# Performance work log

Hardware: AMD Instinct MI355X
Metric: run time of the kernel (lower is better)

The kernel has to match this reference:

```python
import jax, jax.numpy as jnp
import numpy as np

B, S, E, H = 4, 2048, 1024, 16
D = E // H  # head dim = 64


def setup_inputs() -> dict:
    key = jax.random.key(0)
    ks = jax.random.split(key, 5)
    s = 0.02
    return {
        "x": jax.random.normal(ks[0], (B, S, E), dtype=jnp.float32),
        "Wq": jax.random.normal(ks[1], (E, E), dtype=jnp.float32) * s,
        "Wk": jax.random.normal(ks[2], (E, E), dtype=jnp.float32) * s,
        "Wv": jax.random.normal(ks[3], (E, E), dtype=jnp.float32) * s,
        "Wo": jax.random.normal(ks[4], (E, E), dtype=jnp.float32) * s,
        "bo": jnp.zeros((E,), dtype=jnp.float32),
    }


def reference(x, Wq, Wk, Wv, Wo, bo):
    b, s, e = x.shape
    h, d = H, e // H
    # QKV projections -> [b, h, s, d]
    q = (x @ Wq).reshape(b, s, h, d).transpose(0, 2, 1, 3)
    k = (x @ Wk).reshape(b, s, h, d).transpose(0, 2, 1, 3)
    v = (x @ Wv).reshape(b, s, h, d).transpose(0, 2, 1, 3)
    # scores [b, h, s, s], causal mask with -inf, scaled softmax
    a = jnp.einsum('bhqd,bhkd->bhqk', q, k)
    causal = jnp.tril(jnp.ones((s, s), dtype=bool))  # True where allowed
    a = jnp.where(causal, a, -jnp.inf) / jnp.sqrt(jnp.asarray(d, x.dtype))
    a = jax.nn.softmax(a, axis=-1)
    # dropout p=0.0 (identity in eval)
    y = jnp.einsum('bhqk,bhkd->bhqd', a, v)
    y = y.transpose(0, 2, 1, 3).reshape(b, s, e)
    return y @ Wo + bo
```

## Files before the change

kernel.cpp:

```cpp
#include <hip/hip_runtime.h>

typedef __bf16 bf16x8 __attribute__((ext_vector_type(8)));
typedef float f32x4 __attribute__((ext_vector_type(4)));
typedef unsigned short u16x8 __attribute__((ext_vector_type(8)));

#define S_LEN 2048
#define NHEAD 16
#define HDIM  64
#define EMB   1024

__device__ __forceinline__ ushort f2b(float v) {
  union { float f; unsigned u; } x; x.f = v;
  unsigned r = (x.u + 0x7fffu + ((x.u >> 16) & 1u)) >> 16;
  return (ushort)r;
}

__device__ __forceinline__ ushort f2b_trunc(float v) {
  union { float f; unsigned u; } x; x.f = v;
  return (ushort)(x.u >> 16);
}

typedef const __attribute__((address_space(1))) unsigned int* gp1_t;
typedef __attribute__((address_space(3))) unsigned int* lp3_t;
__device__ __forceinline__ void gld16(const ushort* g, const ushort* l) {
  __builtin_amdgcn_global_load_lds((gp1_t)(unsigned long long)(uintptr_t)g,
                                   (lp3_t)(unsigned int)(uintptr_t)l, 16, 0, 0);
}

__device__ __forceinline__ void barf() {
  asm volatile("" ::: "memory");
  __builtin_amdgcn_s_barrier();
  asm volatile("" ::: "memory");
}

__global__ __launch_bounds__(256) void prep_kernel(
    const float* __restrict__ x, const float* __restrict__ W0,
    const float* __restrict__ W1, const float* __restrict__ W2,
    const float* __restrict__ W3, ushort* __restrict__ xb,
    ushort* __restrict__ Wt0, ushort* __restrict__ Wt1,
    ushort* __restrict__ Wt2, ushort* __restrict__ Wt3, float scale0) {
  const int z = blockIdx.z;
  if (z == 4) {
    size_t base = ((size_t)(blockIdx.y * 32 + blockIdx.x)) * 8192 + threadIdx.x * 4;
#pragma unroll
    for (int i = 0; i < 8; ++i) {
      float4 v = *(const float4*)(x + base + i * 1024);
      ushort4 o;
      o.x = f2b(v.x); o.y = f2b(v.y); o.z = f2b(v.z); o.w = f2b(v.w);
      *(ushort4*)(xb + base + i * 1024) = o;
    }
    return;
  }
  __shared__ float t[32][33];
  const float* W = z == 0 ? W0 : (z == 1 ? W1 : (z == 2 ? W2 : W3));
  ushort* Wt = z == 0 ? Wt0 : (z == 1 ? Wt1 : (z == 2 ? Wt2 : Wt3));
  const float scale = z == 0 ? scale0 : 1.0f;
  int k0 = blockIdx.x * 32, n0 = blockIdx.y * 32;
  int c = threadIdx.x & 31, r0 = threadIdx.x >> 5;
#pragma unroll
  for (int i = 0; i < 4; ++i) {
    int r = r0 + i * 8;
    t[r][c] = W[(size_t)(k0 + r) * EMB + n0 + c];
  }
  __syncthreads();
#pragma unroll
  for (int i = 0; i < 4; ++i) {
    int r = r0 + i * 8;
    Wt[(size_t)(n0 + r) * EMB + k0 + c] = f2b(t[c][r] * scale);
  }
}

template <int EPI>
__global__ __launch_bounds__(512, 2) void gemm8_kernel(
    const ushort* __restrict__ A, const ushort* __restrict__ Bt,
    ushort* __restrict__ outQ, ushort* __restrict__ outK, ushort* __restrict__ outVt,
    float* __restrict__ outF, const float* __restrict__ bias) {
  __shared__ ushort lds8[73728];
  const int tid = threadIdx.x;
  const int wave = tid >> 6, lane = tid & 63, ln = lane & 15, quad = lane >> 4;
  const int wm = wave >> 2, wn = wave & 3;
  const long m0 = (long)blockIdx.x * 128, n0 = (long)blockIdx.y * 256;
  constexpr int K = EMB, KT = K / 64;

  const int srow = tid >> 3;
  const int scol = ((tid & 7) ^ (srow & 7)) * 8;
  const ushort* srcA = A + (m0 + srow) * (long)K + scol;
  const ushort* srcB = Bt + (n0 + srow) * (long)K + scol;

#define STG_A(t, s)                                                            \
  do {                                                                         \
    gld16(srcA + (t) * 64,               lds8 + (s) * 8192 + tid * 8);         \
    gld16(srcA + (t) * 64 + 64 * K,      lds8 + (s) * 8192 + 4096 + tid * 8);  \
  } while (0)
#define STG_B(t, s)                                                            \
  do {                                                                         \
    gld16(srcB + (t) * 64,               lds8 + 24576 + (s) * 16384 + tid * 8);         \
    gld16(srcB + (t) * 64 + 64 * K,      lds8 + 24576 + (s) * 16384 + 4096 + tid * 8);  \
    gld16(srcB + (t) * 64 + 128 * K,     lds8 + 24576 + (s) * 16384 + 8192 + tid * 8);  \
    gld16(srcB + (t) * 64 + 192 * K,     lds8 + 24576 + (s) * 16384 + 12288 + tid * 8); \
  } while (0)

  const int sw = (ln & 7) * 8;

#define RD_A(kk, s)                                                            \
  do {                                                                         \
    const ushort* p_ = lds8 + (s) * 8192 + (wm * 64 + ln) * 64 +               \
                       (((kk) * 32 + quad * 8) ^ sw);                          \
    af[0] = *(const bf16x8*)p_;                                                \
    af[1] = *(const bf16x8*)(p_ + 1024);                                       \
    af[2] = *(const bf16x8*)(p_ + 2048);                                       \
    af[3] = *(const bf16x8*)(p_ + 3072);                                       \
  } while (0)
#define RD_B(kk, s)                                                            \
  do {                                                                         \
    const ushort* p_ = lds8 + 24576 + (s) * 16384 + (wn * 64 + ln) * 64 +      \
                       (((kk) * 32 + quad * 8) ^ sw);                          \
    bfr[0] = *(const bf16x8*)p_;                                               \
    bfr[1] = *(const bf16x8*)(p_ + 1024);                                      \
    bfr[2] = *(const bf16x8*)(p_ + 2048);                                      \
    bfr[3] = *(const bf16x8*)(p_ + 3072);                                      \
  } while (0)

#define MM16()                                                                 \
  do {                                                                         \
    _Pragma("unroll") for (int mt = 0; mt < 4; ++mt)                           \
        _Pragma("unroll") for (int nt = 0; nt < 4; ++nt)                       \
            acc[mt][nt] = __builtin_amdgcn_mfma_f32_16x16x32_bf16(             \
                af[mt], bfr[nt], acc[mt][nt], 0, 0, 0);                        \
  } while (0)

  STG_A(0, 0); STG_B(0, 0);
  STG_A(1, 1); STG_B(1, 1);
  asm volatile("s_waitcnt vmcnt(6)" ::: "memory");
  barf();

  f32x4 acc[4][4] = {};
  bf16x8 af[4], bfr[4];

#define TILE(t, s, sn)                                                         \
  do {                                                                         \
    RD_A(0, s); RD_B(0, s);                                                    \
    if ((t) + 2 < KT) STG_A((t) + 2, sn);                                      \
    barf();                                                                    \
    __builtin_amdgcn_s_setprio(1);                                             \
    MM16();                                                                    \
    __builtin_amdgcn_s_setprio(0);                                             \
    barf();                                                                    \
    RD_A(1, s); RD_B(1, s);                                                    \
    if ((t) + 2 < KT) STG_B((t) + 2, sn);                                      \
    barf();                                                                    \
    __builtin_amdgcn_s_setprio(1);                                             \
    MM16();                                                                    \
    __builtin_amdgcn_s_setprio(0);                                             \
    if ((t) + 2 < KT) {                                                        \
      asm volatile("s_waitcnt vmcnt(6)" ::: "memory");                         \
    } else if ((t) + 1 < KT) {                                                 \
      asm volatile("s_waitcnt vmcnt(0)" ::: "memory");                         \
    }                                                                          \
    barf();                                                                    \
  } while (0)

  for (int th = 0; th < 15; th += 3) {
    TILE(th, 0, 2);
    TILE(th + 1, 1, 0);
    TILE(th + 2, 2, 1);
  }
  TILE(15, 0, 2);

  if (EPI == 0) {
    const int sel = (int)(n0 >> 10);
    if (sel == 2) {
#pragma unroll
      for (int mt = 0; mt < 4; ++mt) {
        const long mbase = m0 + wm * 64 + mt * 16 + quad * 4;
        const long bb = mbase >> 11, s = mbase & 2047;
#pragma unroll
        for (int nt = 0; nt < 4; ++nt) {
          const int nn = (int)((n0 & 1023) + wn * 64 + nt * 16 + ln);
          const int h = nn >> 6, d = nn & 63;
          uint2 val;
          val.x = (unsigned)f2b(acc[mt][nt][0]) | ((unsigned)f2b(acc[mt][nt][1]) << 16);
          val.y = (unsigned)f2b(acc[mt][nt][2]) | ((unsigned)f2b(acc[mt][nt][3]) << 16);
          *(uint2*)(outVt + (((bb * NHEAD + h) * (long)HDIM + d) * S_LEN) + s) = val;
        }
      }
    } else {
      ushort* dst = sel == 0 ? outQ : outK;
#pragma unroll
      for (int mt = 0; mt < 4; ++mt) {
#pragma unroll
        for (int nt = 0; nt < 4; ++nt) {
          const int nn = (int)((n0 & 1023) + wn * 64 + nt * 16 + ln);
          const int h = nn >> 6, d = nn & 63;
#pragma unroll
          for (int r = 0; r < 4; ++r) {
            const long m = m0 + wm * 64 + mt * 16 + quad * 4 + r;
            const long bb = m >> 11, s = m & 2047;
            dst[(((bb * NHEAD + h) * S_LEN) + s) * HDIM + d] = f2b(acc[mt][nt][r]);
          }
        }
      }
    }
  } else {
#pragma unroll
    for (int mt = 0; mt < 4; ++mt) {
#pragma unroll
      for (int nt = 0; nt < 4; ++nt) {
        const long n = n0 + wn * 64 + nt * 16 + ln;
        const float bv = bias[n];
#pragma unroll
        for (int r = 0; r < 4; ++r) {
          const long m = m0 + wm * 64 + mt * 16 + quad * 4 + r;
          outF[m * (long)EMB + n] = acc[mt][nt][r] + bv;
        }
      }
    }
  }
#undef TILE
#undef MM16
#undef RD_B
#undef RD_A
#undef STG_B
#undef STG_A
}

__global__ __launch_bounds__(256) void attn_kernel(const ushort* __restrict__ Q,
                                                   const ushort* __restrict__ Kg,
                                                   const ushort* __restrict__ Vt,
                                                   ushort* __restrict__ Y) {
  __shared__ alignas(16) ushort Ks[2][2 * 64 * 32];
  __shared__ alignas(16) ushort Vs[2][2 * 64 * 32];
  __shared__ alignas(16) ushort Ps[4 * 2 * 16 * 72];
  const int tid = threadIdx.x;
  const int wave = tid >> 6, lane = tid & 63, ln = lane & 15, quad = lane >> 4;
  const int bh = blockIdx.x;
  const int qb = 15 - (int)blockIdx.y;
  const int q0 = qb * 128;
  const size_t base = (size_t)bh * S_LEN * HDIM;
  const int ntiles = 2 * qb + 2;

  const u16x8 ob = {0x3F80, 0x3F80, 0x3F80, 0x3F80, 0x3F80, 0x3F80, 0x3F80, 0x3F80};
  const bf16x8 ones = __builtin_bit_cast(bf16x8, ob);

  bf16x8 qf[2][2];
#pragma unroll
  for (int mt = 0; mt < 2; ++mt)
#pragma unroll
    for (int ks2 = 0; ks2 < 2; ++ks2)
      qf[mt][ks2] = *(const bf16x8*)(Q + base + (size_t)(q0 + wave * 32 + mt * 16 + ln) * HDIM +
                                     ks2 * 32 + quad * 8);

  f32x4 acc[2][4] = {};
  f32x4 accl[2] = {};

  const int sr = lane >> 2, sc = (lane & 3) * 8;
  const ushort* KgL = Kg + base + (size_t)(16 * wave + sr) * HDIM + sc;
  const ushort* VgL = Vt + base + (size_t)(16 * wave + sr) * S_LEN + sc;

  {
    ushort* kb = &Ks[0][16 * wave * 32];
    ushort* vb = &Vs[0][16 * wave * 32];
    gld16(KgL, kb);
    gld16(KgL + 32, kb + 2048);
    gld16(VgL, vb);
    gld16(VgL + 32, vb + 2048);
  }
  __syncthreads();

  ushort* Pw0 = Ps + wave * 2304;
  ushort* Pw1 = Pw0 + 1152;
  const int swW = (quad >> 1) << 4;
  const int swR = (ln >> 3) << 4;

  for (int kt = 0; kt < ntiles; ++kt) {
    const int cur = kt & 1;
    const int k0 = kt * 64;
    if (kt + 1 < ntiles) {
      const int nb = cur ^ 1;
      const size_t k1 = (size_t)(k0 + 64);
      ushort* kb = &Ks[nb][16 * wave * 32];
      ushort* vb = &Vs[nb][16 * wave * 32];
      gld16(KgL + k1 * HDIM, kb);
      gld16(KgL + k1 * HDIM + 32, kb + 2048);
      gld16(VgL + k1, vb);
      gld16(VgL + k1 + 32, vb + 2048);
    }
    const ushort* Kc = &Ks[cur][0];
    const ushort* Vc = &Vs[cur][0];
    const int qbase = q0 + wave * 32;

    if (k0 < qbase + 32) {
      f32x4 s0[4] = {}, s1[4] = {};
#pragma unroll
      for (int ks2 = 0; ks2 < 2; ++ks2) {
#pragma unroll
        for (int nt = 0; nt < 4; ++nt) {
          bf16x8 bk = *(const bf16x8*)(Kc + ks2 * 2048 + (nt * 16 + ln) * 32 + quad * 8);
          s0[nt] = __builtin_amdgcn_mfma_f32_16x16x32_bf16(qf[0][ks2], bk, s0[nt], 0, 0, 0);
          s1[nt] = __builtin_amdgcn_mfma_f32_16x16x32_bf16(qf[1][ks2], bk, s1[nt], 0, 0, 0);
        }
      }

      if (k0 + 63 > qbase) {
        const int rowq = qbase + quad * 4;
#pragma unroll
        for (int nt = 0; nt < 4; ++nt)
#pragma unroll
          for (int r = 0; r < 4; ++r) {
            const int key = k0 + nt * 16 + ln;
            if (key > rowq + r) s0[nt][r] = -3.0e38f;
            if (key > rowq + 16 + r) s1[nt][r] = -3.0e38f;
          }
      }

      asm volatile("" ::: "memory");
#pragma unroll
      for (int nt = 0; nt < 4; ++nt) {
#pragma unroll
        for (int r = 0; r < 4; ++r) {
          float p0 = __builtin_amdgcn_exp2f(s0[nt][r]);
          float p1 = __builtin_amdgcn_exp2f(s1[nt][r]);
          const int row = (quad * 4 + r) * 72;
          const int col = (nt * 16 + ln) ^ swW;
          Pw0[row + col] = f2b_trunc(p0);
          Pw1[row + col] = f2b_trunc(p1);
        }
      }
      asm volatile("" ::: "memory");

#pragma unroll
      for (int ks2 = 0; ks2 < 2; ++ks2) {
        const int rcol = (ks2 * 32 + quad * 8) ^ swR;
        bf16x8 ap0 = *(const bf16x8*)(Pw0 + ln * 72 + rcol);
        bf16x8 ap1 = *(const bf16x8*)(Pw1 + ln * 72 + rcol);
        accl[0] = __builtin_amdgcn_mfma_f32_16x16x32_bf16(ap0, ones, accl[0], 0, 0, 0);
        accl[1] = __builtin_amdgcn_mfma_f32_16x16x32_bf16(ap1, ones, accl[1], 0, 0, 0);
#pragma unroll
        for (int t2 = 0; t2 < 4; ++t2) {
          bf16x8 bv = *(const bf16x8*)(Vc + ks2 * 2048 + (t2 * 16 + ln) * 32 + quad * 8);
          acc[0][t2] = __builtin_amdgcn_mfma_f32_16x16x32_bf16(ap0, bv, acc[0][t2], 0, 0, 0);
          acc[1][t2] = __builtin_amdgcn_mfma_f32_16x16x32_bf16(ap1, bv, acc[1][t2], 0, 0, 0);
        }
      }
    }
    __syncthreads();
  }

  const long b = bh >> 4;
  const int h = bh & 15;
#pragma unroll
  for (int mt = 0; mt < 2; ++mt) {
#pragma unroll
    for (int r = 0; r < 4; ++r) {
      float inv = 1.0f / accl[mt][r];
      const int qq = q0 + wave * 32 + mt * 16 + quad * 4 + r;
#pragma unroll
      for (int t2 = 0; t2 < 4; ++t2)
        Y[(((b * S_LEN + qq) * NHEAD) + h) * HDIM + t2 * 16 + ln] = f2b(acc[mt][t2][r] * inv);
    }
  }
}

extern "C" void kernel_launch(void* const* d_in, const int* in_sizes, int n_in,
                              void* d_out, int out_size, void* d_ws, size_t ws_size,
                              hipStream_t stream) {
  const float* x  = (const float*)d_in[0];
  const float* Wq = (const float*)d_in[1];
  const float* Wk = (const float*)d_in[2];
  const float* Wv = (const float*)d_in[3];
  const float* Wo = (const float*)d_in[4];
  const float* bo = (const float*)d_in[5];
  float* out = (float*)d_out;

  const size_t XE = (size_t)8192 * EMB;
  ushort* ws    = (ushort*)d_ws;
  ushort* xb    = ws;
  ushort* Wtqkv = xb + XE;
  ushort* Wto   = Wtqkv + 3 * 1048576;
  ushort* Qb    = Wto + 1048576;
  ushort* Kb    = Qb + XE;
  ushort* Vtb   = Kb + XE;
  ushort* Yb    = xb;

  const float SCALE_Q = 1.4426950408889634f / 8.0f;

  prep_kernel<<<dim3(32, 32, 5), 256, 0, stream>>>(
      x, Wq, Wk, Wv, Wo, xb, Wtqkv, Wtqkv + 1048576, Wtqkv + 2097152, Wto, SCALE_Q);

  gemm8_kernel<0><<<dim3(64, 12), 512, 0, stream>>>(xb, Wtqkv, Qb, Kb, Vtb,
                                                    nullptr, nullptr);
  attn_kernel<<<dim3(64, 16), 256, 0, stream>>>(Qb, Kb, Vtb, Yb);
  gemm8_kernel<1><<<dim3(64, 4), 512, 0, stream>>>(Yb, Wto, nullptr, nullptr,
                                                   nullptr, out, bo);
}
```

Before: 230.6 us.

## Double-buffer GEMM LDS fragments and cut barriers per K-tile

Restructures the GEMM main loop so LDS fragment reads for the next half-tile go into a second register set while MFMAs run on the current one. The four barriers per K-tile drop to one, and global prefetch stores are issued alongside the compute. This targets LDS-read latency and barrier stalls in the projection GEMMs. It costs extra VGPRs for the second fragment buffers and adds a hand-written tail sequence that must match the stage rotation exactly.

Result: no change. 231.2 us (+0.3%).

```diff
diff --git a/kernel.cpp b/kernel.cpp
--- a/kernel.cpp
+++ b/kernel.cpp
@@ -102,70 +102,72 @@
 
   const int sw = (ln & 7) * 8;
 
-#define RD_A(kk, s)                                                            \
+#define RD_A(F, kk, s)                                                         \
   do {                                                                         \
     const ushort* p_ = lds8 + (s) * 8192 + (wm * 64 + ln) * 64 +               \
                        (((kk) * 32 + quad * 8) ^ sw);                          \
-    af[0] = *(const bf16x8*)p_;                                                \
-    af[1] = *(const bf16x8*)(p_ + 1024);                                       \
-    af[2] = *(const bf16x8*)(p_ + 2048);                                       \
-    af[3] = *(const bf16x8*)(p_ + 3072);                                       \
-  } while (0)
-#define RD_B(kk, s)                                                            \
+    F[0] = *(const bf16x8*)p_;                                                 \
+    F[1] = *(const bf16x8*)(p_ + 1024);                                        \
+    F[2] = *(const bf16x8*)(p_ + 2048);                                        \
+    F[3] = *(const bf16x8*)(p_ + 3072);                                        \
+  } while (0)
+#define RD_B(F, kk, s)                                                         \
   do {                                                                         \
     const ushort* p_ = lds8 + 24576 + (s) * 16384 + (wn * 64 + ln) * 64 +      \
                        (((kk) * 32 + quad * 8) ^ sw);                          \
-    bfr[0] = *(const bf16x8*)p_;                                               \
-    bfr[1] = *(const bf16x8*)(p_ + 1024);                                      \
-    bfr[2] = *(const bf16x8*)(p_ + 2048);                                      \
-    bfr[3] = *(const bf16x8*)(p_ + 3072);                                      \
-  } while (0)
-
-#define MM16()                                                                 \
-  do {                                                                         \
+    F[0] = *(const bf16x8*)p_;                                                 \
+    F[1] = *(const bf16x8*)(p_ + 1024);                                        \
+    F[2] = *(const bf16x8*)(p_ + 2048);                                        \
+    F[3] = *(const bf16x8*)(p_ + 3072);                                        \
+  } while (0)
+
+#define MM16(AF, BF)                                                           \
+  do {                                                                         \
+    __builtin_amdgcn_s_setprio(1);                                             \
     _Pragma("unroll") for (int mt = 0; mt < 4; ++mt)                           \
         _Pragma("unroll") for (int nt = 0; nt < 4; ++nt)                       \
             acc[mt][nt] = __builtin_amdgcn_mfma_f32_16x16x32_bf16(             \
-                af[mt], bfr[nt], acc[mt][nt], 0, 0, 0);                        \
-  } while (0)
+                AF[mt], BF[nt], acc[mt][nt], 0, 0, 0);                         \
+    __builtin_amdgcn_s_setprio(0);                                             \
+  } while (0)
+
+  f32x4 acc[4][4] = {};
+  bf16x8 afP[4], bfP[4], afN[4], bfN[4];
 
   STG_A(0, 0); STG_B(0, 0);
   STG_A(1, 1); STG_B(1, 1);
   asm volatile("s_waitcnt vmcnt(6)" ::: "memory");
   barf();
-
-  f32x4 acc[4][4] = {};
-  bf16x8 af[4], bfr[4];
-
-#define TILE(t, s, sn)                                                         \
-  do {                                                                         \
-    RD_A(0, s); RD_B(0, s);                                                    \
-    if ((t) + 2 < KT) STG_A((t) + 2, sn);                                      \
-    barf();                                                                    \
-    __builtin_amdgcn_s_setprio(1);                                             \
-    MM16();                                                                    \
-    __builtin_amdgcn_s_setprio(0);                                             \
-    barf();                                                                    \
-    RD_A(1, s); RD_B(1, s);                                                    \
-    if ((t) + 2 < KT) STG_B((t) + 2, sn);                                      \
-    barf();                                                                    \
-    __builtin_amdgcn_s_setprio(1);                                             \
-    MM16();                                                                    \
-    __builtin_amdgcn_s_setprio(0);                                             \
-    if ((t) + 2 < KT) {                                                        \
-      asm volatile("s_waitcnt vmcnt(6)" ::: "memory");                         \
-    } else if ((t) + 1 < KT) {                                                 \
-      asm volatile("s_waitcnt vmcnt(0)" ::: "memory");                         \
-    }                                                                          \
-    barf();                                                                    \
-  } while (0)
-
-  for (int th = 0; th < 15; th += 3) {
-    TILE(th, 0, 2);
-    TILE(th + 1, 1, 0);
-    TILE(th + 2, 2, 1);
-  }
-  TILE(15, 0, 2);
+  RD_A(afP, 0, 0); RD_B(bfP, 0, 0);
+
+#define TILE_FULL(t, s, s1, s2)                                                \
+  do {                                                                         \
+    STG_A((t) + 2, s2);                                                        \
+    RD_A(afN, 1, s); RD_B(bfN, 1, s);                                          \
+    MM16(afP, bfP);                               \
+    STG_B((t) + 2, s2);                                                        \
+    asm volatile("s_waitcnt vmcnt(6) lgkmcnt(0)" ::: "memory");                \
+    barf();                               \
+    RD_A(afP, 0, s1); RD_B(bfP, 0, s1);                        \
+    MM16(afN, bfN);                               \
+  } while (0)
+
+  for (int th = 0; th < 12; th += 3) {
+    TILE_FULL(th, 0, 1, 2);
+    TILE_FULL(th + 1, 1, 2, 0);
+    TILE_FULL(th + 2, 2, 0, 1);
+  }
+  TILE_FULL(12, 0, 1, 2);
+  TILE_FULL(13, 1, 2, 0);
+  RD_A(afN, 1, 2); RD_B(bfN, 1, 2);
+  MM16(afP, bfP);
+  asm volatile("s_waitcnt vmcnt(0) lgkmcnt(0)" ::: "memory");
+  barf();
+  RD_A(afP, 0, 0); RD_B(bfP, 0, 0);
+  MM16(afN, bfN);
+  RD_A(afN, 1, 0); RD_B(bfN, 1, 0);
+  MM16(afP, bfP);
+  MM16(afN, bfN);
 
   if (EPI == 0) {
     const int sel = (int)(n0 >> 10);
@@ -216,7 +218,7 @@
       }
     }
   }
-#undef TILE
+#undef TILE_FULL
 #undef MM16
 #undef RD_B
 #undef RD_A
```
